# Performance work log

Measured on AMD Instinct MI355X. Metric: run time of the kernel, lower is better.

The kernel has to match this reference:

```python
import jax, jax.numpy as jnp
import numpy as np

ROUTING_ITERATIONS = 3
EPS = 1e-8


def squash(s):
    # standard CapsNet squash along the last (channels_per_unit) axis
    sq = jnp.sum(s * s, axis=-1, keepdims=True)
    return (sq / (1.0 + sq)) * s / jnp.sqrt(sq + EPS)


def setup_inputs() -> dict:
    key = jax.random.key(0)
    k1, k2 = jax.random.split(key)
    # inputs: (batch, input_channels, input_units)
    inputs = jax.random.normal(k1, (32, 8, 1152), dtype=jnp.float32)
    # weights: (input_units, num_units, input_channels, channels_per_unit)
    weights = jax.random.normal(k2, (1152, 10, 8, 16), dtype=jnp.float32)
    return {"inputs": inputs, "weights": weights}


def reference(inputs, weights):
    # (B, C, U) -> (B, U, C)
    votes = jnp.transpose(inputs, (0, 2, 1))
    # broadcast to (B, U, N, C, D): elementwise product as in the torch code
    pondered = weights[None, :, :, :, :] * votes[:, :, None, :, None]
    logits = jnp.zeros_like(pondered)
    out = pondered  # placeholder; overwritten in first iteration
    for _ in range(ROUTING_ITERATIONS):
        couplings = jax.nn.softmax(logits, axis=-1)
        out = squash(couplings * pondered)
        logits = logits + pondered * out  # agreement update
    # (B, U, N, C, D) -> (B, N, U, C, D)
    return jnp.transpose(out, (0, 2, 1, 3, 4))
```

## Files before the change

kernel.cpp:

```cpp
#include <hip/hip_runtime.h>

#define BB 32
#define UU 1152
#define NN 10
#define CC 8
#define DD 16
#define EPS 1e-8f


__device__ __forceinline__ float rcp_fast(float x) { return __builtin_amdgcn_rcpf(x); }
__device__ __forceinline__ float rsq_fast(float x) { return __builtin_amdgcn_rsqf(x); }

__device__ __forceinline__ float quad_sum(float x) {
    float y = __int_as_float(
        __builtin_amdgcn_update_dpp(0, __float_as_int(x), 0xB1, 0xF, 0xF, true));
    x += y;
    y = __int_as_float(
        __builtin_amdgcn_update_dpp(0, __float_as_int(x), 0x4E, 0xF, 0xF, true));
    return x + y;
}

__global__ __launch_bounds__(256) void caps_route_kernel(
    const float* __restrict__ inputs,
    const float* __restrict__ weights,
    float* __restrict__ out)
{
    int t = blockIdx.x * blockDim.x + threadIdx.x;
    int sub = t & 3;
    int g   = t >> 2;

    int c  = g & 7;
    int g2 = g >> 3;
    int u  = g2 % UU;
    int g3 = g2 / UU;
    int n  = g3 % NN;
    int b  = g3 / NN;

    float v = inputs[(b * CC + c) * UU + u];

    const float* wp = weights + (((u * NN + n) * CC + c) * DD) + sub * 4;
    float4 w4 = *reinterpret_cast<const float4*>(wp);

    float p[4];
    p[0] = w4.x * v; p[1] = w4.y * v; p[2] = w4.z * v; p[3] = w4.w * v;

    float logits[4];
    {
        float q0 = p[0] * p[0], q1 = p[1] * p[1];
        float q2 = p[2] * p[2], q3 = p[3] * p[3];
        float sqr = quad_sum((q0 + q1) + (q2 + q3));
        float sq = sqr * (1.0f / 256.0f);
        float scale = sq * rcp_fast(1.0f + sq) * rsq_fast(sq + EPS);
        float kk = scale * (1.0f / 16.0f);
        logits[0] = kk * q0; logits[1] = kk * q1;
        logits[2] = kk * q2; logits[3] = kk * q3;
    }

    {
        float e0 = __expf(logits[0]), e1 = __expf(logits[1]);
        float e2 = __expf(logits[2]), e3 = __expf(logits[3]);
        float sum = quad_sum((e0 + e1) + (e2 + e3));
        float t0 = e0 * p[0], t1 = e1 * p[1], t2 = e2 * p[2], t3 = e3 * p[3];
        float sqt = quad_sum((t0 * t0 + t1 * t1) + (t2 * t2 + t3 * t3));
        float inv = rcp_fast(sum);
        float sq = sqt * inv * inv;
        float k = sq * rcp_fast(1.0f + sq) * rsq_fast(sq + EPS) * inv;
        logits[0] = fmaf(k * p[0], t0, logits[0]);
        logits[1] = fmaf(k * p[1], t1, logits[1]);
        logits[2] = fmaf(k * p[2], t2, logits[2]);
        logits[3] = fmaf(k * p[3], t3, logits[3]);
    }

    {
        float e0 = __expf(logits[0]), e1 = __expf(logits[1]);
        float e2 = __expf(logits[2]), e3 = __expf(logits[3]);
        float sum = quad_sum((e0 + e1) + (e2 + e3));
        float t0 = e0 * p[0], t1 = e1 * p[1], t2 = e2 * p[2], t3 = e3 * p[3];
        float sqt = quad_sum((t0 * t0 + t1 * t1) + (t2 * t2 + t3 * t3));
        float inv = rcp_fast(sum);
        float sq = sqt * inv * inv;
        float k = sq * rcp_fast(1.0f + sq) * rsq_fast(sq + EPS) * inv;

        float* op = out + ((((b * NN + n) * UU + u) * CC + c) * DD) + sub * 4;
        float4 r;
        r.x = k * t0; r.y = k * t1; r.z = k * t2; r.w = k * t3;
        *reinterpret_cast<float4*>(op) = r;
    }
}

extern "C" void kernel_launch(void* const* d_in, const int* in_sizes, int n_in,
                              void* d_out, int out_size, void* d_ws, size_t ws_size,
                              hipStream_t stream) {
    const float* inputs  = (const float*)d_in[0];
    const float* weights = (const float*)d_in[1];
    float* out = (float*)d_out;

    const long long total = (long long)BB * NN * UU * CC * 4;
    const int block = 256;
    const int grid = (int)(total / block);
    caps_route_kernel<<<grid, block, 0, stream>>>(inputs, weights, out);
}
```

Before: 50.27 us.

## Loop over units per thread, use exp2 with folded log2e, nontemporal stores

Each thread now handles all 10 output units for one (b,u,c,sub), looping over n. This reuses the input load and index math across units and shrinks the grid tenfold. The exponentials are switched to a hardware exp2 with the 1/ln2 factor folded into the logit scale. Output is written with nontemporal stores to avoid polluting the cache. Fewer threads in flight lowers parallelism available to hide memory latency on this store-bound kernel.

```diff
diff --git a/kernel.cpp b/kernel.cpp
--- a/kernel.cpp
+++ b/kernel.cpp
@@ -6,10 +6,19 @@
 #define CC 8
 #define DD 16
 #define EPS 1e-8f
+#define INV_LN2 1.44269504088896341f
 
+
+typedef float f32x4 __attribute__((ext_vector_type(4)));
 
 __device__ __forceinline__ float rcp_fast(float x) { return __builtin_amdgcn_rcpf(x); }
 __device__ __forceinline__ float rsq_fast(float x) { return __builtin_amdgcn_rsqf(x); }
+
+#if __has_builtin(__builtin_amdgcn_exp2f)
+__device__ __forceinline__ float exp2_fast(float x) { return __builtin_amdgcn_exp2f(x); }
+#else
+__device__ __forceinline__ float exp2_fast(float x) { return __expf(x * 0.6931471805599453f); }
+#endif
 
 __device__ __forceinline__ float quad_sum(float x) {
     float y = __int_as_float(
@@ -28,63 +37,55 @@
     int t = blockIdx.x * blockDim.x + threadIdx.x;
     int sub = t & 3;
     int g   = t >> 2;
-
-    int c  = g & 7;
-    int g2 = g >> 3;
-    int u  = g2 % UU;
-    int g3 = g2 / UU;
-    int n  = g3 % NN;
-    int b  = g3 / NN;
+    int c   = g & 7;
+    int g2  = g >> 3;
+    int u   = g2 % UU;
+    int b   = g2 / UU;
 
     float v = inputs[(b * CC + c) * UU + u];
 
-    const float* wp = weights + (((u * NN + n) * CC + c) * DD) + sub * 4;
-    float4 w4 = *reinterpret_cast<const float4*>(wp);
+    const float* wbase = weights + (u * NN * CC + c) * DD + sub * 4;
+    float*       obase = out + ((b * NN * UU + u) * CC + c) * DD + sub * 4;
 
-    float p[4];
-    p[0] = w4.x * v; p[1] = w4.y * v; p[2] = w4.z * v; p[3] = w4.w * v;
+    #pragma unroll 2
+    for (int n = 0; n < NN; ++n) {
+        f32x4 w4 = *reinterpret_cast<const f32x4*>(wbase + n * (CC * DD));
+        float p0 = w4.x * v, p1 = w4.y * v, p2 = w4.z * v, p3 = w4.w * v;
 
-    float logits[4];
-    {
-        float q0 = p[0] * p[0], q1 = p[1] * p[1];
-        float q2 = p[2] * p[2], q3 = p[3] * p[3];
+        float q0 = p0 * p0, q1 = p1 * p1, q2 = p2 * p2, q3 = p3 * p3;
         float sqr = quad_sum((q0 + q1) + (q2 + q3));
-        float sq = sqr * (1.0f / 256.0f);
-        float scale = sq * rcp_fast(1.0f + sq) * rsq_fast(sq + EPS);
-        float kk = scale * (1.0f / 16.0f);
-        logits[0] = kk * q0; logits[1] = kk * q1;
-        logits[2] = kk * q2; logits[3] = kk * q3;
-    }
+        float sq0 = sqr * (1.0f / 256.0f);
+        float scale0 = sq0 * rcp_fast(1.0f + sq0) * rsq_fast(sq0 + EPS);
+        float kk = scale0 * (INV_LN2 / 16.0f);
+        float L0 = kk * q0, L1 = kk * q1, L2 = kk * q2, L3 = kk * q3;
 
-    {
-        float e0 = __expf(logits[0]), e1 = __expf(logits[1]);
-        float e2 = __expf(logits[2]), e3 = __expf(logits[3]);
-        float sum = quad_sum((e0 + e1) + (e2 + e3));
-        float t0 = e0 * p[0], t1 = e1 * p[1], t2 = e2 * p[2], t3 = e3 * p[3];
-        float sqt = quad_sum((t0 * t0 + t1 * t1) + (t2 * t2 + t3 * t3));
-        float inv = rcp_fast(sum);
-        float sq = sqt * inv * inv;
-        float k = sq * rcp_fast(1.0f + sq) * rsq_fast(sq + EPS) * inv;
-        logits[0] = fmaf(k * p[0], t0, logits[0]);
-        logits[1] = fmaf(k * p[1], t1, logits[1]);
-        logits[2] = fmaf(k * p[2], t2, logits[2]);
-        logits[3] = fmaf(k * p[3], t3, logits[3]);
-    }
+        {
+            float e0 = exp2_fast(L0), e1 = exp2_fast(L1);
+            float e2 = exp2_fast(L2), e3 = exp2_fast(L3);
+            float sum = quad_sum((e0 + e1) + (e2 + e3));
+            float t0 = e0 * p0, t1 = e1 * p1, t2 = e2 * p2, t3 = e3 * p3;
+            float sqt = quad_sum((t0 * t0 + t1 * t1) + (t2 * t2 + t3 * t3));
+            float inv = rcp_fast(sum);
+            float sq = sqt * inv * inv;
+            float k = sq * rcp_fast(1.0f + sq) * rsq_fast(sq + EPS) * inv * INV_LN2;
+            L0 = fmaf(k * p0, t0, L0); L1 = fmaf(k * p1, t1, L1);
+            L2 = fmaf(k * p2, t2, L2); L3 = fmaf(k * p3, t3, L3);
+        }
 
-    {
-        float e0 = __expf(logits[0]), e1 = __expf(logits[1]);
-        float e2 = __expf(logits[2]), e3 = __expf(logits[3]);
-        float sum = quad_sum((e0 + e1) + (e2 + e3));
-        float t0 = e0 * p[0], t1 = e1 * p[1], t2 = e2 * p[2], t3 = e3 * p[3];
-        float sqt = quad_sum((t0 * t0 + t1 * t1) + (t2 * t2 + t3 * t3));
-        float inv = rcp_fast(sum);
-        float sq = sqt * inv * inv;
-        float k = sq * rcp_fast(1.0f + sq) * rsq_fast(sq + EPS) * inv;
-
-        float* op = out + ((((b * NN + n) * UU + u) * CC + c) * DD) + sub * 4;
-        float4 r;
-        r.x = k * t0; r.y = k * t1; r.z = k * t2; r.w = k * t3;
-        *reinterpret_cast<float4*>(op) = r;
+        {
+            float e0 = exp2_fast(L0), e1 = exp2_fast(L1);
+            float e2 = exp2_fast(L2), e3 = exp2_fast(L3);
+            float sum = quad_sum((e0 + e1) + (e2 + e3));
+            float t0 = e0 * p0, t1 = e1 * p1, t2 = e2 * p2, t3 = e3 * p3;
+            float sqt = quad_sum((t0 * t0 + t1 * t1) + (t2 * t2 + t3 * t3));
+            float inv = rcp_fast(sum);
+            float sq = sqt * inv * inv;
+            float k = sq * rcp_fast(1.0f + sq) * rsq_fast(sq + EPS) * inv;
+            f32x4 r;
+            r.x = k * t0; r.y = k * t1; r.z = k * t2; r.w = k * t3;
+            __builtin_nontemporal_store(
+                r, reinterpret_cast<f32x4*>(obase + n * (UU * CC * DD)));
+        }
     }
 }
 
@@ -95,7 +96,7 @@
     const float* weights = (const float*)d_in[1];
     float* out = (float*)d_out;
 
-    const long long total = (long long)BB * NN * UU * CC * 4;
+    const long long total = (long long)BB * UU * CC * 4;
     const int block = 256;
     const int grid = (int)(total / block);
     caps_route_kernel<<<grid, block, 0, stream>>>(inputs, weights, out);
```

New measurement: 46.31 us. -7.9%, faster.
